# Performance work log

Hardware: AMD Instinct MI355X
Metric: run time of the kernel (lower is better)

Reference implementation:

```python
import jax, jax.numpy as jnp
import numpy as np
import math

D_MODEL = 1024
D_STATE = 16
D_CONV = 4
EXPAND = 2
D_INNER = EXPAND * D_MODEL  # 2048
DT_RANK = 64
B_SZ = 2
L_SEQ = 1024


def setup_inputs() -> dict:
    key = jax.random.key(0)
    ks = jax.random.split(key, 10)
    x = jax.random.normal(ks[0], (B_SZ, L_SEQ, D_MODEL), dtype=jnp.float32)
    in_proj_w = jax.random.normal(ks[1], (2 * D_INNER, D_MODEL), dtype=jnp.float32) * (1.0 / math.sqrt(D_MODEL))
    conv_w = jax.random.normal(ks[2], (D_INNER, 1, D_CONV), dtype=jnp.float32) * (1.0 / math.sqrt(D_CONV))
    conv_b = jax.random.normal(ks[3], (D_INNER,), dtype=jnp.float32) * 0.01
    x_proj_w = jax.random.normal(ks[4], (DT_RANK + 2 * D_STATE, D_INNER), dtype=jnp.float32) * (1.0 / math.sqrt(D_INNER))
    dt_init_std = DT_RANK ** (-0.5)
    dt_proj_w = jax.random.uniform(ks[5], (D_INNER, DT_RANK), dtype=jnp.float32, minval=-dt_init_std, maxval=dt_init_std)
    dt = jnp.exp(jax.random.uniform(ks[6], (D_INNER,), dtype=jnp.float32) * (math.log(0.1) - math.log(0.001)) + math.log(0.001))
    dt = jnp.clip(dt, 1e-4, None)
    dt_proj_b = dt + jnp.log(-jnp.expm1(-dt))
    A_log = jnp.log(jnp.tile(jnp.arange(1, D_STATE + 1, dtype=jnp.float32)[None, :], (D_INNER, 1)))
    D = jnp.ones((D_INNER,), dtype=jnp.float32)
    out_proj_w = jax.random.normal(ks[7], (D_MODEL, D_INNER), dtype=jnp.float32) * (1.0 / math.sqrt(D_INNER))
    return {"x": x, "in_proj_w": in_proj_w, "conv_w": conv_w, "conv_b": conv_b,
            "x_proj_w": x_proj_w, "dt_proj_w": dt_proj_w, "dt_proj_b": dt_proj_b,
            "A_log": A_log, "D": D, "out_proj_w": out_proj_w}


def _mamba_forward(x, in_proj_w, conv_w, conv_b, x_proj_w, dt_proj_w, dt_proj_b, A_log, D, out_proj_w):
    B, L, _ = x.shape
    # input projection -> x, z each [B, L, Di]
    xz = jnp.einsum('bld,ed->ble', x, in_proj_w)
    xs, z = jnp.split(xz, 2, axis=-1)
    # causal depthwise conv along L (torch pads K-1 both sides then trims -> left pad only)
    xc = jnp.transpose(xs, (0, 2, 1))  # [B, Di, L]
    xc = jax.lax.conv_general_dilated(
        xc, conv_w, window_strides=(1,), padding=[(D_CONV - 1, 0)],
        feature_group_count=D_INNER, dimension_numbers=('NCH', 'OIH', 'NCH'))
    xc = xc + conv_b[None, :, None]
    xs = jnp.transpose(xc, (0, 2, 1))  # [B, L, Di]
    xs = jax.nn.silu(xs)
    # SSM parameters
    A = -jnp.exp(A_log)  # [Di, N]
    dbc = jnp.einsum('bld,ed->ble', xs, x_proj_w)
    delta_r = dbc[..., :DT_RANK]
    Bm = dbc[..., DT_RANK:DT_RANK + D_STATE]       # [B, L, N]
    Cm = dbc[..., DT_RANK + D_STATE:]              # [B, L, N]
    delta = jnp.einsum('blr,dr->bld', delta_r, dt_proj_w)
    delta = jax.nn.softplus(delta + dt_proj_b)     # [B, L, Di]
    # selective scan: h_t = exp(delta*A)*h_{t-1} + delta*B*x
    dA = jnp.exp(delta[..., None] * A)                          # [B, L, Di, N]
    dBx = (delta * xs)[..., None] * Bm[:, :, None, :]           # [B, L, Di, N]
    dA_t = jnp.moveaxis(dA, 1, 0)    # [L, B, Di, N]
    dBx_t = jnp.moveaxis(dBx, 1, 0)
    C_t = jnp.moveaxis(Cm, 1, 0)     # [L, B, N]
    h0 = jnp.zeros((B, D_INNER, D_STATE), dtype=xs.dtype)

    def step(h, inp):
        da, bx, c = inp
        h = da * h + bx
        y = jnp.einsum('bdn,bn->bd', h, c)
        return h, y

    _, ys = jax.lax.scan(step, h0, (dA_t, dBx_t, C_t))
    y = jnp.moveaxis(ys, 0, 1)       # [B, L, Di]
    y = y + D * xs
    # gating and output projection
    out = y * jax.nn.silu(z)
    return jnp.einsum('bld,od->blo', out, out_proj_w)


def reference(x, in_proj_w, conv_w, conv_b, x_proj_w, dt_proj_w, dt_proj_b, A_log, D, out_proj_w):
    return _mamba_forward(x, in_proj_w, conv_w, conv_b, x_proj_w, dt_proj_w, dt_proj_b, A_log, D, out_proj_w)
```

## Files before the change

kernel.cpp:

```cpp
#include <hip/hip_runtime.h>
#include <hip/hip_bf16.h>

typedef __attribute__((ext_vector_type(8))) short short8;
typedef __attribute__((ext_vector_type(4))) float f32x4;
typedef __hip_bfloat16 bf16;

#define D_MODEL 1024
#define D_INNER 2048
#define DT_RANK 64
#define D_STATE 16
#define B_SZ 2
#define L_SEQ 1024
#define NSEG 32
#define SL 32

__device__ __forceinline__ float b2f(bf16 x){ return __bfloat162float(x); }
__device__ __forceinline__ bf16  f2b(float x){ return __float2bfloat16(x); }

__device__ __forceinline__ void cvt_store8(bf16* dst, const float* s){
  union { short8 v; bf16 e[8]; } u;
  #pragma unroll
  for (int i = 0; i < 8; i++) u.e[i] = f2b(s[i]);
  *(short8*)dst = u.v;
}

__device__ __forceinline__ void gl_lds16(const bf16* g, bf16* l){
  __builtin_amdgcn_global_load_lds((const __attribute__((address_space(1))) unsigned int*)g,
                                   (__attribute__((address_space(3))) unsigned int*)l, 16, 0, 0);
}

__global__ __launch_bounds__(256) void cvt5_k(const float* s0, bf16* d0, int c0,
                                              const float* s1, bf16* d1, int c1,
                                              const float* s2, bf16* d2, int c2,
                                              const float* s3, bf16* d3, int c3,
                                              const float* s4, bf16* d4, int c4)
{
  int i = blockIdx.x * 256 + threadIdx.x;
  const float* s; bf16* d; int off;
  if      (i < c0) { s = s0; d = d0; off = i; }
  else if (i < c1) { s = s1; d = d1; off = i - c0; }
  else if (i < c2) { s = s2; d = d2; off = i - c1; }
  else if (i < c3) { s = s3; d = d3; off = i - c2; }
  else if (i < c4) { s = s4; d = d4; off = i - c3; }
  else return;
  float b[8];
  *(float4*)&b[0] = *(const float4*)(s + (size_t)off * 8);
  *(float4*)&b[4] = *(const float4*)(s + (size_t)off * 8 + 4);
  cvt_store8(d + (size_t)off * 8, b);
}

template<int MODE, int JT>
__global__ __launch_bounds__(256) void gemm_glds(const bf16* __restrict__ A,
                                                 const bf16* __restrict__ B,
                                                 void* __restrict__ Cout,
                                                 int M, int N, int K)
{
  constexpr int BN = JT * 32;
  constexpr int AI = 4;
  constexpr int BI = BN / 32;
  __shared__ bf16 As[128 * 64];
  __shared__ bf16 Bs[BN * 64];

  const int gx = gridDim.x;
  const int nwg = gx * gridDim.y;
  const int flat = blockIdx.y * gx + blockIdx.x;
  const int swz = (flat & 7) * (nwg >> 3) + (flat >> 3);
  const int bm = (swz / gx) * 128, bn = (swz % gx) * BN;

  const int tid  = threadIdx.x;
  const int lane = tid & 63, wave = tid >> 6;
  const int wm = (wave & 1) * 64, wn = (wave >> 1) * (JT * 16);
  const int r = lane & 15, q = lane >> 4;
  const int rx = r & 7;

  const bf16* asrc[AI];
  #pragma unroll
  for (int i = 0; i < AI; i++) {
    int c = i * 256 + tid;
    int row = c >> 3, sl = (c & 7) ^ (row & 7);
    asrc[i] = A + (size_t)(bm + row) * K + sl * 8;
  }
  const bf16* bsrc[BI];
  #pragma unroll
  for (int i = 0; i < BI; i++) {
    int c = i * 256 + tid;
    int row = c >> 3, sl = (c & 7) ^ (row & 7);
    bsrc[i] = B + (size_t)(bn + row) * K + sl * 8;
  }

  f32x4 acc[4][JT];
  #pragma unroll
  for (int i = 0; i < 4; i++)
    #pragma unroll
    for (int j = 0; j < JT; j++) acc[i][j] = (f32x4){0.f,0.f,0.f,0.f};

  for (int k0 = 0; k0 < K; k0 += 64) {
    #pragma unroll
    for (int i = 0; i < AI; i++)
      gl_lds16(asrc[i] + k0, &As[(i * 256 + tid) * 8]);
    #pragma unroll
    for (int i = 0; i < BI; i++)
      gl_lds16(bsrc[i] + k0, &Bs[(i * 256 + tid) * 8]);
    __syncthreads();
    #pragma unroll
    for (int ks = 0; ks < 2; ks++) {
      short8 af[4], bfr[JT];
      #pragma unroll
      for (int i = 0; i < 4; i++)
        af[i]  = *(const short8*)&As[(wm + i*16 + r) * 64 + ((q + ks*4) ^ rx) * 8];
      #pragma unroll
      for (int j = 0; j < JT; j++)
        bfr[j] = *(const short8*)&Bs[(wn + j*16 + r) * 64 + ((q + ks*4) ^ rx) * 8];
      #pragma unroll
      for (int j = 0; j < JT; j++)
        #pragma unroll
        for (int i = 0; i < 4; i++)
          acc[i][j] = __builtin_amdgcn_mfma_f32_16x16x32_bf16(af[i], bfr[j], acc[i][j], 0, 0, 0);
    }
    __syncthreads();
  }

  #pragma unroll
  for (int i = 0; i < 4; i++)
    #pragma unroll
    for (int j = 0; j < JT; j++)
      #pragma unroll
      for (int t = 0; t < 4; t++) {
        int row = bm + wm + i*16 + q*4 + t;
        int col = bn + wn + j*16 + r;
        float v = acc[i][j][t];
        if (MODE == 0) ((float*)Cout)[(size_t)row * N + col] = v;
        else           ((bf16*)Cout)[(size_t)row * N + col] = f2b(v);
      }
}

__global__ __launch_bounds__(256) void gemm_dt(const bf16* __restrict__ A,
                                               const bf16* __restrict__ W,
                                               float* __restrict__ Cout,
                                               const float* __restrict__ bias,
                                               int M, int N)
{
  __shared__ __align__(16) float stg[4][16][68];
  const int lane = threadIdx.x & 63, wave = threadIdx.x >> 6;
  const int ntg  = N >> 6;
  const int task = blockIdx.x * 4 + wave;
  const int mt   = task / ntg;
  const int ng   = task - mt * ntg;
  const int r = lane & 15, q = lane >> 4;

  const bf16* pa = A + (size_t)(mt*16 + r) * DT_RANK + q*8;
  short8 a0 = *(const short8*)pa;
  short8 a1 = *(const short8*)(pa + 32);

  #pragma unroll
  for (int j = 0; j < 4; j++) {
    const bf16* pb = W + (size_t)(ng*64 + j*16 + r) * DT_RANK + q*8;
    short8 b0 = *(const short8*)pb;
    short8 b1 = *(const short8*)(pb + 32);
    f32x4 c = {0.f,0.f,0.f,0.f};
    c = __builtin_amdgcn_mfma_f32_16x16x32_bf16(a0, b0, c, 0, 0, 0);
    c = __builtin_amdgcn_mfma_f32_16x16x32_bf16(a1, b1, c, 0, 0, 0);
    float bv = bias[ng*64 + j*16 + r];
    #pragma unroll
    for (int t = 0; t < 4; t++) {
      float xv = c[t] + bv;
      float sp = (xv > 20.f) ? xv : log1pf(__expf(xv));
      stg[wave][q*4 + t][j*16 + r] = sp;
    }
  }
  {
    int row = lane >> 2, q4 = lane & 3;
    const float* src = &stg[wave][row][q4 * 16];
    float4 w0 = *(const float4*)(src);
    float4 w1 = *(const float4*)(src + 4);
    float4 w2 = *(const float4*)(src + 8);
    float4 w3 = *(const float4*)(src + 12);
    float* gdst = Cout + (size_t)(mt*16 + row) * N + ng*64 + q4*16;
    *(float4*)(gdst)      = w0;
    *(float4*)(gdst + 4)  = w1;
    *(float4*)(gdst + 8)  = w2;
    *(float4*)(gdst + 12) = w3;
  }
}

__global__ __launch_bounds__(256) void gemm_xproj(const bf16* __restrict__ A,
                                                  const bf16* __restrict__ W,
                                                  float* __restrict__ dbc,
                                                  bf16* __restrict__ dr)
{
  const int K = D_INNER;
  const int lane = threadIdx.x & 63, wave = threadIdx.x >> 6;
  const int mt = blockIdx.y * 4 + wave;
  const int nt = blockIdx.x;
  const int r = lane & 15, q = lane >> 4;
  const bf16* pa = A + (size_t)(mt*16 + r) * K + q*8;
  const bf16* pb = W + (size_t)(nt*16 + r) * K + q*8;
  f32x4 a0 = {0.f,0.f,0.f,0.f}, a1 = a0, a2 = a0, a3 = a0;
  for (int k0 = 0; k0 < K; k0 += 128) {
    short8 x0 = *(const short8*)(pa + k0);
    short8 w0 = *(const short8*)(pb + k0);
    short8 x1 = *(const short8*)(pa + k0 + 32);
    short8 w1 = *(const short8*)(pb + k0 + 32);
    short8 x2 = *(const short8*)(pa + k0 + 64);
    short8 w2 = *(const short8*)(pb + k0 + 64);
    short8 x3 = *(const short8*)(pa + k0 + 96);
    short8 w3 = *(const short8*)(pb + k0 + 96);
    a0 = __builtin_amdgcn_mfma_f32_16x16x32_bf16(x0, w0, a0, 0, 0, 0);
    a1 = __builtin_amdgcn_mfma_f32_16x16x32_bf16(x1, w1, a1, 0, 0, 0);
    a2 = __builtin_amdgcn_mfma_f32_16x16x32_bf16(x2, w2, a2, 0, 0, 0);
    a3 = __builtin_amdgcn_mfma_f32_16x16x32_bf16(x3, w3, a3, 0, 0, 0);
  }
  f32x4 acc = (a0 + a1) + (a2 + a3);
  #pragma unroll
  for (int t = 0; t < 4; t++) {
    int row = mt*16 + q*4 + t;
    int col = nt*16 + r;
    dbc[(size_t)row * 96 + col] = acc[t];
    if (col < DT_RANK) dr[(size_t)row * DT_RANK + col] = f2b(acc[t]);
  }
}

__global__ __launch_bounds__(256) void conv_silu_k(const bf16* __restrict__ xz,
                                                   const float* __restrict__ cw,
                                                   const float* __restrict__ cb,
                                                   bf16* __restrict__ xs_b)
{
  int idx = blockIdx.x * 256 + threadIdx.x;
  int dg = idx & (D_INNER/8 - 1);
  int bl = idx >> 8;
  int l  = bl & (L_SEQ - 1);
  int d0 = dg * 8;
  const float4* cw4 = (const float4*)cw;
  float4 w[8];
  #pragma unroll
  for (int i = 0; i < 8; i++) w[i] = cw4[d0 + i];
  float acc[8];
  #pragma unroll
  for (int i = 0; i < 8; i++) acc[i] = cb[d0 + i];
  #pragma unroll
  for (int j = 0; j < 4; ++j) {
    int lp = l - 3 + j;
    if (lp >= 0) {
      short8 v = *(const short8*)(xz + (size_t)(bl - 3 + j) * (2*D_INNER) + d0);
      #pragma unroll
      for (int i = 0; i < 8; i++)
        acc[i] += ((const float*)&w[i])[j] * b2f(((const bf16*)&v)[i]);
    }
  }
  float o[8];
  #pragma unroll
  for (int i = 0; i < 8; i++) o[i] = acc[i] / (1.f + __expf(-acc[i]));
  cvt_store8(xs_b + (size_t)idx * 8, o);
}

__device__ __forceinline__ bool an_is_int(const float* An){
  bool f = true;
  #pragma unroll
  for (int n = 0; n < 16; n++) f = f & (fabsf(An[n] + (float)(n+1)) < 1e-3f);
  return f;
}

__global__ __launch_bounds__(256) void scan_pass1(const float* __restrict__ delta,
                                                  const bf16* __restrict__ xs,
                                                  const float* __restrict__ dbc,
                                                  const float* __restrict__ A_log,
                                                  float* __restrict__ hseg,
                                                  float* __restrict__ Stot)
{
  __shared__ float bcs[SL][32];
  const int d   = blockIdx.x * 256 + threadIdx.x;
  const int seg = blockIdx.y, b = blockIdx.z;
  for (int i = threadIdx.x; i < SL*32; i += 256) {
    int l = i >> 5, c = i & 31;
    bcs[l][c] = dbc[((size_t)b*L_SEQ + seg*SL + l)*96 + DT_RANK + c];
  }
  __syncthreads();
  float An[16], h[16];
  #pragma unroll
  for (int n = 0; n < 16; n++) { An[n] = -__expf(A_log[d*16 + n]); h[n] = 0.f; }
  float S = 0.f;
  if (an_is_int(An)) {
    for (int li = 0; li < SL; ++li) {
      size_t bl = (size_t)b * L_SEQ + seg*SL + li;
      float dv = delta[bl*D_INNER + d];
      float xv = b2f(xs[bl*D_INNER + d]);
      S += dv;
      float dx = dv * xv;
      float q = __expf(-dv), w = 1.f;
      #pragma unroll
      for (int n = 0; n < 16; n++) {
        w *= q;
        h[n] = w * h[n] + dx * bcs[li][n];
      }
    }
  } else {
    for (int li = 0; li < SL; ++li) {
      size_t bl = (size_t)b * L_SEQ + seg*SL + li;
      float dv = delta[bl*D_INNER + d];
      float xv = b2f(xs[bl*D_INNER + d]);
      S += dv;
      float dx = dv * xv;
      #pragma unroll
      for (int n = 0; n < 16; n++)
        h[n] = __expf(dv * An[n]) * h[n] + dx * bcs[li][n];
    }
  }
  float* hp = hseg + (((size_t)seg*B_SZ + b)*D_INNER + d) * 16;
  #pragma unroll
  for (int n = 0; n < 16; n++) hp[n] = h[n];
  Stot[((size_t)seg*B_SZ + b)*D_INNER + d] = S;
}

__global__ __launch_bounds__(256) void scan_pass3(const float* __restrict__ delta,
                                                  const bf16* __restrict__ xs,
                                                  const float* __restrict__ dbc,
                                                  const float* __restrict__ A_log,
                                                  const float* __restrict__ hseg,
                                                  const float* __restrict__ Stot,
                                                  const bf16* __restrict__ xz,
                                                  const float* __restrict__ Dw,
                                                  bf16* __restrict__ outin)
{
  __shared__ float bcs[SL][32];
  const int d   = blockIdx.x * 256 + threadIdx.x;
  const int seg = blockIdx.y, b = blockIdx.z;
  for (int i = threadIdx.x; i < SL*32; i += 256) {
    int l = i >> 5, c = i & 31;
    bcs[l][c] = dbc[((size_t)b*L_SEQ + seg*SL + l)*96 + DT_RANK + c];
  }
  __syncthreads();
  float An[16], h[16];
  #pragma unroll
  for (int n = 0; n < 16; n++) { An[n] = -__expf(A_log[d*16 + n]); h[n] = 0.f; }
  const bool fast = an_is_int(An);

  if (fast) {
    for (int s = 0; s < seg; ++s) {
      size_t base = ((size_t)s*B_SZ + b)*D_INNER + d;
      float St = Stot[base];
      const float4* hp4 = (const float4*)(hseg + base*16);
      float4 e0 = hp4[0], e1 = hp4[1], e2 = hp4[2], e3 = hp4[3];
      float he[16] = {e0.x,e0.y,e0.z,e0.w, e1.x,e1.y,e1.z,e1.w,
                      e2.x,e2.y,e2.z,e2.w, e3.x,e3.y,e3.z,e3.w};
      float qs = __expf(-St), w = 1.f;
      #pragma unroll
      for (int n = 0; n < 16; n++) {
        w *= qs;
        h[n] = w * h[n] + he[n];
      }
    }
  } else {
    for (int s = 0; s < seg; ++s) {
      size_t base = ((size_t)s*B_SZ + b)*D_INNER + d;
      float St = Stot[base];
      const float4* hp4 = (const float4*)(hseg + base*16);
      float4 e0 = hp4[0], e1 = hp4[1], e2 = hp4[2], e3 = hp4[3];
      float he[16] = {e0.x,e0.y,e0.z,e0.w, e1.x,e1.y,e1.z,e1.w,
                      e2.x,e2.y,e2.z,e2.w, e3.x,e3.y,e3.z,e3.w};
      #pragma unroll
      for (int n = 0; n < 16; n++)
        h[n] = __expf(An[n]*St) * h[n] + he[n];
    }
  }

  const float Dv = Dw[d];
  if (fast) {
    for (int li = 0; li < SL; ++li) {
      size_t bl = (size_t)b * L_SEQ + seg*SL + li;
      float dv = delta[bl*D_INNER + d];
      float xv = b2f(xs[bl*D_INNER + d]);
      float dx = dv * xv;
      float q = __expf(-dv), w = 1.f;
      float y = 0.f;
      #pragma unroll
      for (int n = 0; n < 16; n++) {
        w *= q;
        h[n] = w * h[n] + dx * bcs[li][n];
        y   += h[n] * bcs[li][16 + n];
      }
      y += Dv * xv;
      float z = b2f(xz[bl*(size_t)(2*D_INNER) + D_INNER + d]);
      float g = z / (1.f + __expf(-z));
      outin[bl*D_INNER + d] = f2b(y * g);
    }
  } else {
    for (int li = 0; li < SL; ++li) {
      size_t bl = (size_t)b * L_SEQ + seg*SL + li;
      float dv = delta[bl*D_INNER + d];
      float xv = b2f(xs[bl*D_INNER + d]);
      float dx = dv * xv;
      float y = 0.f;
      #pragma unroll
      for (int n = 0; n < 16; n++) {
        h[n] = __expf(dv * An[n]) * h[n] + dx * bcs[li][n];
        y   += h[n] * bcs[li][16 + n];
      }
      y += Dv * xv;
      float z = b2f(xz[bl*(size_t)(2*D_INNER) + D_INNER + d]);
      float g = z / (1.f + __expf(-z));
      outin[bl*D_INNER + d] = f2b(y * g);
    }
  }
}

extern "C" void kernel_launch(void* const* d_in, const int* in_sizes, int n_in,
                              void* d_out, int out_size, void* d_ws, size_t ws_size,
                              hipStream_t stream)
{
  const float* x      = (const float*)d_in[0];
  const float* in_w   = (const float*)d_in[1];
  const float* conv_w = (const float*)d_in[2];
  const float* conv_b = (const float*)d_in[3];
  const float* xp_w   = (const float*)d_in[4];
  const float* dt_w   = (const float*)d_in[5];
  const float* dt_b   = (const float*)d_in[6];
  const float* A_log  = (const float*)d_in[7];
  const float* Dw     = (const float*)d_in[8];
  const float* out_w  = (const float*)d_in[9];
  float* out = (float*)d_out;

  char* p = (char*)d_ws;
  bf16*  xz    = (bf16*)p;  p += (size_t)B_SZ*L_SEQ*2*D_INNER*2;
  bf16*  xs_b  = (bf16*)p;  p += (size_t)B_SZ*L_SEQ*D_INNER*2;
  float* dbc   = (float*)p; p += (size_t)B_SZ*L_SEQ*96*4;
  bf16*  dr    = (bf16*)p;  p += (size_t)B_SZ*L_SEQ*DT_RANK*2;
  float* delta = (float*)p; p += (size_t)B_SZ*L_SEQ*D_INNER*4;
  float* Stot  = (float*)p; p += (size_t)NSEG*B_SZ*D_INNER*4;
  bf16*  outin = (bf16*)p;  p += (size_t)B_SZ*L_SEQ*D_INNER*2;
  bf16*  xp_wb = (bf16*)p;  p += (size_t)(DT_RANK+2*D_STATE)*D_INNER*2;
  bf16*  dt_wb = (bf16*)p;  p += (size_t)D_INNER*DT_RANK*2;
  bf16*  ow_b  = (bf16*)p;  p += (size_t)D_MODEL*D_INNER*2;
  char* u = p;
  bf16*  xb    = (bf16*)u;
  bf16*  in_wb = (bf16*)(u + (size_t)B_SZ*L_SEQ*D_MODEL*2);
  float* hseg  = (float*)u;
  p += (size_t)B_SZ*L_SEQ*(D_MODEL + 2*D_INNER)*2;

  const int M = B_SZ * L_SEQ;

  cvt5_k<<<4256, 256, 0, stream>>>(x, xb, 262144,
                                   in_w, in_wb, 786432,
                                   xp_w, xp_wb, 811008,
                                   dt_w, dt_wb, 827392,
                                   out_w, ow_b, 1089536);
  gemm_glds<2,2><<<dim3(2*D_INNER/64, M/128), 256, 0, stream>>>(xb, in_wb, xz, M, 2*D_INNER, D_MODEL);
  conv_silu_k<<<(M*D_INNER/8)/256, 256, 0, stream>>>(xz, conv_w, conv_b, xs_b);
  gemm_xproj<<<dim3(6, M/64), 256, 0, stream>>>(xs_b, xp_wb, dbc, dr);
  gemm_dt<<<(M/16)*(D_INNER/64)/4, 256, 0, stream>>>(dr, dt_wb, delta, dt_b, M, D_INNER);
  scan_pass1<<<dim3(D_INNER/256, NSEG, B_SZ), 256, 0, stream>>>(delta, xs_b, dbc, A_log, hseg, Stot);
  scan_pass3<<<dim3(D_INNER/256, NSEG, B_SZ), 256, 0, stream>>>(delta, xs_b, dbc, A_log, hseg, Stot, xz, Dw, outin);
  gemm_glds<0,2><<<dim3(D_MODEL/64, M/128), 256, 0, stream>>>(outin, ow_b, out, M, D_MODEL, D_INNER);
}
```

Baseline: 247.4 us.

## Fuse dt projection and softplus into both scan passes, drop delta buffer

Removes the standalone gemm_dt kernel and the fp32 delta buffer in global memory. Each scan block now computes its 32x256 delta tile with MFMA from the low-rank dr rows and the dt weights, applies softplus, and keeps the result in shared memory. This saves one launch plus writing and twice re-reading a 16 MB delta array. In exchange the delta GEMM and the softplus transcendentals are computed twice (once per pass), and each block uses more LDS, which may reduce occupancy.

```diff
diff --git a/kernel.cpp b/kernel.cpp
--- a/kernel.cpp
+++ b/kernel.cpp
@@ -132,55 +132,6 @@
         if (MODE == 0) ((float*)Cout)[(size_t)row * N + col] = v;
         else           ((bf16*)Cout)[(size_t)row * N + col] = f2b(v);
       }
-}
-
-__global__ __launch_bounds__(256) void gemm_dt(const bf16* __restrict__ A,
-                                               const bf16* __restrict__ W,
-                                               float* __restrict__ Cout,
-                                               const float* __restrict__ bias,
-                                               int M, int N)
-{
-  __shared__ __align__(16) float stg[4][16][68];
-  const int lane = threadIdx.x & 63, wave = threadIdx.x >> 6;
-  const int ntg  = N >> 6;
-  const int task = blockIdx.x * 4 + wave;
-  const int mt   = task / ntg;
-  const int ng   = task - mt * ntg;
-  const int r = lane & 15, q = lane >> 4;
-
-  const bf16* pa = A + (size_t)(mt*16 + r) * DT_RANK + q*8;
-  short8 a0 = *(const short8*)pa;
-  short8 a1 = *(const short8*)(pa + 32);
-
-  #pragma unroll
-  for (int j = 0; j < 4; j++) {
-    const bf16* pb = W + (size_t)(ng*64 + j*16 + r) * DT_RANK + q*8;
-    short8 b0 = *(const short8*)pb;
-    short8 b1 = *(const short8*)(pb + 32);
-    f32x4 c = {0.f,0.f,0.f,0.f};
-    c = __builtin_amdgcn_mfma_f32_16x16x32_bf16(a0, b0, c, 0, 0, 0);
-    c = __builtin_amdgcn_mfma_f32_16x16x32_bf16(a1, b1, c, 0, 0, 0);
-    float bv = bias[ng*64 + j*16 + r];
-    #pragma unroll
-    for (int t = 0; t < 4; t++) {
-      float xv = c[t] + bv;
-      float sp = (xv > 20.f) ? xv : log1pf(__expf(xv));
-      stg[wave][q*4 + t][j*16 + r] = sp;
-    }
-  }
-  {
-    int row = lane >> 2, q4 = lane & 3;
-    const float* src = &stg[wave][row][q4 * 16];
-    float4 w0 = *(const float4*)(src);
-    float4 w1 = *(const float4*)(src + 4);
-    float4 w2 = *(const float4*)(src + 8);
-    float4 w3 = *(const float4*)(src + 12);
-    float* gdst = Cout + (size_t)(mt*16 + row) * N + ng*64 + q4*16;
-    *(float4*)(gdst)      = w0;
-    *(float4*)(gdst + 4)  = w1;
-    *(float4*)(gdst + 8)  = w2;
-    *(float4*)(gdst + 12) = w3;
-  }
 }
 
 __global__ __launch_bounds__(256) void gemm_xproj(const bf16* __restrict__ A,
@@ -260,7 +211,52 @@
   return f;
 }
 
-__global__ __launch_bounds__(256) void scan_pass1(const float* __restrict__ delta,
+__device__ __forceinline__ void delta_tile_mfma(const bf16* __restrict__ dr,
+                                                const bf16* __restrict__ dtw,
+                                                const float* __restrict__ dt_b,
+                                                int b, int seg, int d0,
+                                                bf16 (*dr_s)[64],
+                                                float (*delta_s)[257])
+{
+  const int tid  = threadIdx.x;
+  const int lane = tid & 63, wave = tid >> 6;
+  const int r = lane & 15, q = lane >> 4;
+  const int rx = r & 7;
+  {
+    int row = tid >> 3, slot = tid & 7;
+    const bf16* src = dr + (size_t)(b*L_SEQ + seg*SL + row) * DT_RANK
+                         + ((slot ^ (row & 7)) * 8);
+    gl_lds16(src, &dr_s[0][0] + tid * 8);
+  }
+  __syncthreads();
+  #pragma unroll
+  for (int rt = 0; rt < 2; rt++) {
+    short8 a0 = *(const short8*)&dr_s[rt*16 + r][((q    ) ^ rx) * 8];
+    short8 a1 = *(const short8*)&dr_s[rt*16 + r][((4 + q) ^ rx) * 8];
+    #pragma unroll
+    for (int ct = 0; ct < 4; ct++) {
+      int dcol = d0 + wave*64 + ct*16 + r;
+      const bf16* pb = dtw + (size_t)dcol * DT_RANK + q*8;
+      short8 b0 = *(const short8*)pb;
+      short8 b1 = *(const short8*)(pb + 32);
+      f32x4 c = {0.f,0.f,0.f,0.f};
+      c = __builtin_amdgcn_mfma_f32_16x16x32_bf16(a0, b0, c, 0, 0, 0);
+      c = __builtin_amdgcn_mfma_f32_16x16x32_bf16(a1, b1, c, 0, 0, 0);
+      float bv = dt_b[dcol];
+      #pragma unroll
+      for (int t = 0; t < 4; t++) {
+        float xv = c[t] + bv;
+        float sp = (xv > 20.f) ? xv : log1pf(__expf(xv));
+        delta_s[rt*16 + q*4 + t][wave*64 + ct*16 + r] = sp;
+      }
+    }
+  }
+  __syncthreads();
+}
+
+__global__ __launch_bounds__(256) void scan_pass1(const bf16* __restrict__ dr,
+                                                  const bf16* __restrict__ dtw,
+                                                  const float* __restrict__ dt_b,
                                                   const bf16* __restrict__ xs,
                                                   const float* __restrict__ dbc,
                                                   const float* __restrict__ A_log,
@@ -268,13 +264,17 @@
                                                   float* __restrict__ Stot)
 {
   __shared__ float bcs[SL][32];
-  const int d   = blockIdx.x * 256 + threadIdx.x;
+  __shared__ bf16 dr_s[SL][64];
+  __shared__ float delta_s[SL][257];
+  const int tid = threadIdx.x;
+  const int d   = blockIdx.x * 256 + tid;
   const int seg = blockIdx.y, b = blockIdx.z;
-  for (int i = threadIdx.x; i < SL*32; i += 256) {
+  for (int i = tid; i < SL*32; i += 256) {
     int l = i >> 5, c = i & 31;
     bcs[l][c] = dbc[((size_t)b*L_SEQ + seg*SL + l)*96 + DT_RANK + c];
   }
-  __syncthreads();
+  delta_tile_mfma(dr, dtw, dt_b, b, seg, blockIdx.x * 256, dr_s, delta_s);
+
   float An[16], h[16];
   #pragma unroll
   for (int n = 0; n < 16; n++) { An[n] = -__expf(A_log[d*16 + n]); h[n] = 0.f; }
@@ -282,7 +282,7 @@
   if (an_is_int(An)) {
     for (int li = 0; li < SL; ++li) {
       size_t bl = (size_t)b * L_SEQ + seg*SL + li;
-      float dv = delta[bl*D_INNER + d];
+      float dv = delta_s[li][tid];
       float xv = b2f(xs[bl*D_INNER + d]);
       S += dv;
       float dx = dv * xv;
@@ -296,7 +296,7 @@
   } else {
     for (int li = 0; li < SL; ++li) {
       size_t bl = (size_t)b * L_SEQ + seg*SL + li;
-      float dv = delta[bl*D_INNER + d];
+      float dv = delta_s[li][tid];
       float xv = b2f(xs[bl*D_INNER + d]);
       S += dv;
       float dx = dv * xv;
@@ -311,7 +311,9 @@
   Stot[((size_t)seg*B_SZ + b)*D_INNER + d] = S;
 }
 
-__global__ __launch_bounds__(256) void scan_pass3(const float* __restrict__ delta,
+__global__ __launch_bounds__(256) void scan_pass3(const bf16* __restrict__ dr,
+                                                  const bf16* __restrict__ dtw,
+                                                  const float* __restrict__ dt_b,
                                                   const bf16* __restrict__ xs,
                                                   const float* __restrict__ dbc,
                                                   const float* __restrict__ A_log,
@@ -322,13 +324,17 @@
                                                   bf16* __restrict__ outin)
 {
   __shared__ float bcs[SL][32];
-  const int d   = blockIdx.x * 256 + threadIdx.x;
+  __shared__ bf16 dr_s[SL][64];
+  __shared__ float delta_s[SL][257];
+  const int tid = threadIdx.x;
+  const int d   = blockIdx.x * 256 + tid;
   const int seg = blockIdx.y, b = blockIdx.z;
-  for (int i = threadIdx.x; i < SL*32; i += 256) {
+  for (int i = tid; i < SL*32; i += 256) {
     int l = i >> 5, c = i & 31;
     bcs[l][c] = dbc[((size_t)b*L_SEQ + seg*SL + l)*96 + DT_RANK + c];
   }
-  __syncthreads();
+  delta_tile_mfma(dr, dtw, dt_b, b, seg, blockIdx.x * 256, dr_s, delta_s);
+
   float An[16], h[16];
   #pragma unroll
   for (int n = 0; n < 16; n++) { An[n] = -__expf(A_log[d*16 + n]); h[n] = 0.f; }
@@ -367,7 +373,7 @@
   if (fast) {
     for (int li = 0; li < SL; ++li) {
       size_t bl = (size_t)b * L_SEQ + seg*SL + li;
-      float dv = delta[bl*D_INNER + d];
+      float dv = delta_s[li][tid];
       float xv = b2f(xs[bl*D_INNER + d]);
       float dx = dv * xv;
       float q = __expf(-dv), w = 1.f;
@@ -386,7 +392,7 @@
   } else {
     for (int li = 0; li < SL; ++li) {
       size_t bl = (size_t)b * L_SEQ + seg*SL + li;
-      float dv = delta[bl*D_INNER + d];
+      float dv = delta_s[li][tid];
       float xv = b2f(xs[bl*D_INNER + d]);
       float dx = dv * xv;
       float y = 0.f;
@@ -424,7 +430,6 @@
   bf16*  xs_b  = (bf16*)p;  p += (size_t)B_SZ*L_SEQ*D_INNER*2;
   float* dbc   = (float*)p; p += (size_t)B_SZ*L_SEQ*96*4;
   bf16*  dr    = (bf16*)p;  p += (size_t)B_SZ*L_SEQ*DT_RANK*2;
-  float* delta = (float*)p; p += (size_t)B_SZ*L_SEQ*D_INNER*4;
   float* Stot  = (float*)p; p += (size_t)NSEG*B_SZ*D_INNER*4;
   bf16*  outin = (bf16*)p;  p += (size_t)B_SZ*L_SEQ*D_INNER*2;
   bf16*  xp_wb = (bf16*)p;  p += (size_t)(DT_RANK+2*D_STATE)*D_INNER*2;
@@ -446,8 +451,7 @@
   gemm_glds<2,2><<<dim3(2*D_INNER/64, M/128), 256, 0, stream>>>(xb, in_wb, xz, M, 2*D_INNER, D_MODEL);
   conv_silu_k<<<(M*D_INNER/8)/256, 256, 0, stream>>>(xz, conv_w, conv_b, xs_b);
   gemm_xproj<<<dim3(6, M/64), 256, 0, stream>>>(xs_b, xp_wb, dbc, dr);
-  gemm_dt<<<(M/16)*(D_INNER/64)/4, 256, 0, stream>>>(dr, dt_wb, delta, dt_b, M, D_INNER);
-  scan_pass1<<<dim3(D_INNER/256, NSEG, B_SZ), 256, 0, stream>>>(delta, xs_b, dbc, A_log, hseg, Stot);
-  scan_pass3<<<dim3(D_INNER/256, NSEG, B_SZ), 256, 0, stream>>>(delta, xs_b, dbc, A_log, hseg, Stot, xz, Dw, outin);
+  scan_pass1<<<dim3(D_INNER/256, NSEG, B_SZ), 256, 0, stream>>>(dr, dt_wb, dt_b, xs_b, dbc, A_log, hseg, Stot);
+  scan_pass3<<<dim3(D_INNER/256, NSEG, B_SZ), 256, 0, stream>>>(dr, dt_wb, dt_b, xs_b, dbc, A_log, hseg, Stot, xz, Dw, outin);
   gemm_glds<0,2><<<dim3(D_MODEL/64, M/128), 256, 0, stream>>>(outin, ow_b, out, M, D_MODEL, D_INNER);
 }
```

Result: slower. 256.9 us (+3.8%).
